# Kernel optimization log

Hardware: AMD Instinct MI355X
Metric: run time of the kernel (lower is better)

The kernel has to match this reference:

```python
import jax, jax.numpy as jnp
import numpy as np

N_QUBITS = 4
N_LAYERS = 3
SHORT_W = 2048
LONG_W = 8192
BATCH = 2048


def _conv1d(x, w, b, pad):
    # x: [B, Cin, L], w: [Cout, Cin, K]
    y = jax.lax.conv_general_dilated(x, w, window_strides=(1,), padding=[(pad, pad)],
                                     dimension_numbers=("NCH", "OIH", "NCH"))
    return y + b[None, :, None]


def _ry_mat(t):
    c, s = jnp.cos(t / 2), jnp.sin(t / 2)
    return jnp.stack([jnp.stack([c, -s]), jnp.stack([s, c])]).astype(jnp.complex64)


def _rz_mat(a):
    return jnp.diag(jnp.stack([jnp.exp(-0.5j * a), jnp.exp(0.5j * a)])).astype(jnp.complex64)


def _rot_mat(phi, theta, omega):
    # PennyLane Rot(phi, theta, omega) = RZ(omega) @ RY(theta) @ RZ(phi)
    return _rz_mat(omega) @ _ry_mat(theta) @ _rz_mat(phi)


def _apply_1q(state, U, wire):
    state = jnp.tensordot(U, state, axes=((1,), (wire,)))
    return jnp.moveaxis(state, 0, wire)


def _apply_cnot(state, c, t):
    s0 = jax.lax.index_in_dim(state, 0, axis=c, keepdims=True)
    s1 = jax.lax.index_in_dim(state, 1, axis=c, keepdims=True)
    s1 = jnp.flip(s1, axis=t)
    return jnp.concatenate([s0, s1], axis=c)


def _circuit(x, w):
    # x: [4] real features, w: [3, 4, 3] StronglyEntanglingLayers weights
    state = jnp.zeros((2,) * N_QUBITS, jnp.complex64).at[(0,) * N_QUBITS].set(1.0)
    for i in range(N_QUBITS):
        state = _apply_1q(state, _ry_mat(jnp.pi * x[i]), i)
    for l in range(N_LAYERS):
        r = (l % (N_QUBITS - 1)) + 1  # default PennyLane ranges: 1,2,3
        for i in range(N_QUBITS):
            state = _apply_1q(state, _rot_mat(w[l, i, 0], w[l, i, 1], w[l, i, 2]), i)
        for i in range(N_QUBITS):
            state = _apply_cnot(state, i, (i + r) % N_QUBITS)
    probs = jnp.abs(state) ** 2
    zs = []
    for i in range(N_QUBITS):
        p = probs.sum(axis=tuple(a for a in range(N_QUBITS) if a != i))
        zs.append(p[0] - p[1])  # <PauliZ_i>
    return jnp.stack(zs)


def setup_inputs() -> dict:
    key = jax.random.key(0)
    ks = jax.random.split(key, 13)
    d = {}
    d["xs"] = jax.random.normal(ks[0], (BATCH, 1, SHORT_W), jnp.float32)
    d["xl"] = jax.random.normal(ks[1], (BATCH, 1, LONG_W), jnp.float32)
    d["cs_conv_w"] = jax.random.normal(ks[2], (8, 1, 3), jnp.float32) * 0.3
    d["cs_conv_b"] = jax.random.normal(ks[3], (8,), jnp.float32) * 0.1
    d["cs_lin_w"] = jax.random.normal(ks[4], (2, 8 * SHORT_W), jnp.float32) * (1.0 / np.sqrt(8 * SHORT_W))
    d["cs_lin_b"] = jax.random.normal(ks[5], (2,), jnp.float32) * 0.1
    d["cl_conv_w"] = jax.random.normal(ks[6], (8, 1, 5), jnp.float32) * 0.3
    d["cl_conv_b"] = jax.random.normal(ks[7], (8,), jnp.float32) * 0.1
    d["cl_lin_w"] = jax.random.normal(ks[8], (2, 8 * LONG_W // 2), jnp.float32) * (1.0 / np.sqrt(8 * LONG_W // 2))
    d["cl_lin_b"] = jax.random.normal(ks[9], (2,), jnp.float32) * 0.1
    d["rw"] = jax.random.normal(ks[10], (N_LAYERS, N_QUBITS, 3), jnp.float32)
    d["fc_w"] = jax.random.normal(ks[11], (1, N_QUBITS), jnp.float32) * 0.5
    d["fc_b"] = jax.random.normal(ks[12], (1,), jnp.float32) * 0.1
    return d


def reference(xs, xl, cs_conv_w, cs_conv_b, cs_lin_w, cs_lin_b,
              cl_conv_w, cl_conv_b, cl_lin_w, cl_lin_b, rw, fc_w, fc_b):
    B = xs.shape[0]
    # short branch: conv(k=3,p=1) -> relu -> flatten -> linear
    hs = jax.nn.relu(_conv1d(xs, cs_conv_w, cs_conv_b, 1)).reshape(B, -1)
    fs = hs @ cs_lin_w.T + cs_lin_b  # [B, 2]
    # long branch: conv(k=5,p=2) -> relu -> maxpool(2) -> flatten -> linear
    hl = jax.nn.relu(_conv1d(xl, cl_conv_w, cl_conv_b, 2))
    hl = hl.reshape(B, 8, LONG_W // 2, 2).max(axis=-1).reshape(B, -1)
    fl = hl @ cl_lin_w.T + cl_lin_b  # [B, 2]
    f = jnp.concatenate([fs, fl], axis=1)  # [B, 4]
    # original detaches features before the quantum circuit
    f = jax.lax.stop_gradient(f)
    rw_c = jax.lax.stop_gradient(rw)
    qo = jax.vmap(lambda x: _circuit(x, rw_c))(f).astype(jnp.float32)  # [B, 4]
    return qo @ fc_w.T + fc_b  # [B, 1]
```

## Files before the change

kernel.cpp:

```cpp
#include <hip/hip_runtime.h>
#include <math.h>

namespace {
constexpr int kB  = 2048;
constexpr int kSW = 2048;
constexpr int kLW = 8192;
constexpr int kLP = kLW / 2;
constexpr int kROWS = 4;
constexpr int kNBLK = 3072;
}

__device__ __forceinline__ void pin(float& x) { asm volatile("" : "+v"(x)); }

__device__ __forceinline__ void long_quarter(
    int blk, int q, const float* __restrict__ xl, const float* __restrict__ cw,
    const float* __restrict__ cb, const float* __restrict__ lw,
    float* __restrict__ partL) {
  __shared__ float red[kROWS][2][4];
  const int tid = threadIdx.x;
  const int b0 = blk * kROWS;

  float wgt[8][5], bias[8];
#pragma unroll
  for (int c = 0; c < 8; ++c) {
#pragma unroll
    for (int k = 0; k < 5; ++k) wgt[c][k] = cw[c * 5 + k];
    bias[c] = cb[c];
  }

  const int p0 = q * 1024 + tid * 4;
  const int s  = 2 * p0;

  float la[8][4], lbv[8][4];
#pragma unroll
  for (int c = 0; c < 8; ++c) {
    float4 a4 = *reinterpret_cast<const float4*>(lw + (size_t)c * kLP + p0);
    float4 b4 = *reinterpret_cast<const float4*>(lw + (size_t)(8 + c) * kLP + p0);
    la[c][0] = a4.x; la[c][1] = a4.y; la[c][2] = a4.z; la[c][3] = a4.w;
    lbv[c][0] = b4.x; lbv[c][1] = b4.y; lbv[c][2] = b4.z; lbv[c][3] = b4.w;
  }
#pragma unroll
  for (int c = 0; c < 8; ++c)
#pragma unroll
    for (int u = 0; u < 4; ++u) { pin(la[c][u]); pin(lbv[c][u]); }

  float acc[kROWS][2];
#pragma unroll
  for (int r = 0; r < kROWS; ++r) { acc[r][0] = 0.f; acc[r][1] = 0.f; }

#pragma unroll
  for (int g = 0; g < 2; ++g) {
    float w[2][12];
#pragma unroll
    for (int r = 0; r < 2; ++r) {
      const float* x = xl + (size_t)(b0 + g * 2 + r) * kLW;
      float2 hm = (p0 > 0) ? *reinterpret_cast<const float2*>(x + s - 2)
                           : make_float2(0.f, 0.f);
      float4 f0 = *reinterpret_cast<const float4*>(x + s);
      float4 f1 = *reinterpret_cast<const float4*>(x + s + 4);
      float2 f2 = (s + 8 < kLW) ? *reinterpret_cast<const float2*>(x + s + 8)
                                : make_float2(0.f, 0.f);
      w[r][0] = hm.x; w[r][1] = hm.y;
      w[r][2] = f0.x; w[r][3] = f0.y; w[r][4] = f0.z; w[r][5] = f0.w;
      w[r][6] = f1.x; w[r][7] = f1.y; w[r][8] = f1.z; w[r][9] = f1.w;
      w[r][10] = f2.x; w[r][11] = f2.y;
    }
#pragma unroll
    for (int r = 0; r < 2; ++r)
#pragma unroll
      for (int k = 0; k < 12; ++k) pin(w[r][k]);

#pragma unroll
    for (int c = 0; c < 8; ++c) {
#pragma unroll
      for (int r = 0; r < 2; ++r) {
        const int rr = g * 2 + r;
#pragma unroll
        for (int u = 0; u < 4; ++u) {
          float v0 = fmaf(wgt[c][0], w[r][2 * u + 0],
                     fmaf(wgt[c][1], w[r][2 * u + 1],
                     fmaf(wgt[c][2], w[r][2 * u + 2],
                     fmaf(wgt[c][3], w[r][2 * u + 3],
                     fmaf(wgt[c][4], w[r][2 * u + 4], bias[c])))));
          float v1 = fmaf(wgt[c][0], w[r][2 * u + 1],
                     fmaf(wgt[c][1], w[r][2 * u + 2],
                     fmaf(wgt[c][2], w[r][2 * u + 3],
                     fmaf(wgt[c][3], w[r][2 * u + 4],
                     fmaf(wgt[c][4], w[r][2 * u + 5], bias[c])))));
          const float m = fmaxf(fmaxf(v0, v1), 0.f);
          acc[rr][0] = fmaf(m, la[c][u], acc[rr][0]);
          acc[rr][1] = fmaf(m, lbv[c][u], acc[rr][1]);
        }
      }
    }
  }

#pragma unroll
  for (int r = 0; r < kROWS; ++r)
#pragma unroll
    for (int o = 0; o < 2; ++o) {
      float a = acc[r][o];
#pragma unroll
      for (int off = 32; off > 0; off >>= 1) a += __shfl_down(a, off);
      if ((tid & 63) == 0) red[r][o][tid >> 6] = a;
    }
  __syncthreads();
  if (tid < kROWS * 2) {
    const int r = tid >> 1, o = tid & 1;
    partL[(size_t)q * kB * 2 + (size_t)(b0 + r) * 2 + o] =
        red[r][o][0] + red[r][o][1] + red[r][o][2] + red[r][o][3];
  }
}

__device__ __forceinline__ void short_half(
    int blk, int h, const float* __restrict__ xs, const float* __restrict__ cw,
    const float* __restrict__ cb, const float* __restrict__ lw,
    float* __restrict__ partS) {
  __shared__ float red[kROWS][2][4];
  const int tid = threadIdx.x;
  const int b0 = blk * kROWS;

  float wgt[8][3], bias[8];
#pragma unroll
  for (int c = 0; c < 8; ++c) {
#pragma unroll
    for (int k = 0; k < 3; ++k) wgt[c][k] = cw[c * 3 + k];
    bias[c] = cb[c];
  }

  const int p0 = h * 1024 + tid * 4;

  float la[8][4], lbv[8][4];
#pragma unroll
  for (int c = 0; c < 8; ++c) {
    float4 a4 = *reinterpret_cast<const float4*>(lw + (size_t)c * kSW + p0);
    float4 b4 = *reinterpret_cast<const float4*>(lw + (size_t)(8 + c) * kSW + p0);
    la[c][0] = a4.x; la[c][1] = a4.y; la[c][2] = a4.z; la[c][3] = a4.w;
    lbv[c][0] = b4.x; lbv[c][1] = b4.y; lbv[c][2] = b4.z; lbv[c][3] = b4.w;
  }
#pragma unroll
  for (int c = 0; c < 8; ++c)
#pragma unroll
    for (int u = 0; u < 4; ++u) { pin(la[c][u]); pin(lbv[c][u]); }

  float w[kROWS][6];
#pragma unroll
  for (int r = 0; r < kROWS; ++r) {
    const float* x = xs + (size_t)(b0 + r) * kSW;
    float xm = (p0 > 0) ? x[p0 - 1] : 0.f;
    float4 f0 = *reinterpret_cast<const float4*>(x + p0);
    float xp = (p0 + 4 < kSW) ? x[p0 + 4] : 0.f;
    w[r][0] = xm;
    w[r][1] = f0.x; w[r][2] = f0.y; w[r][3] = f0.z; w[r][4] = f0.w;
    w[r][5] = xp;
  }
#pragma unroll
  for (int r = 0; r < kROWS; ++r)
#pragma unroll
    for (int k = 0; k < 6; ++k) pin(w[r][k]);

  float acc[kROWS][2];
#pragma unroll
  for (int r = 0; r < kROWS; ++r) { acc[r][0] = 0.f; acc[r][1] = 0.f; }

#pragma unroll
  for (int c = 0; c < 8; ++c) {
#pragma unroll
    for (int r = 0; r < kROWS; ++r) {
#pragma unroll
      for (int u = 0; u < 4; ++u) {
        float v = fmaf(wgt[c][0], w[r][u],
                  fmaf(wgt[c][1], w[r][u + 1],
                  fmaf(wgt[c][2], w[r][u + 2], bias[c])));
        const float m = fmaxf(v, 0.f);
        acc[r][0] = fmaf(m, la[c][u], acc[r][0]);
        acc[r][1] = fmaf(m, lbv[c][u], acc[r][1]);
      }
    }
  }

#pragma unroll
  for (int r = 0; r < kROWS; ++r)
#pragma unroll
    for (int o = 0; o < 2; ++o) {
      float a = acc[r][o];
#pragma unroll
      for (int off = 32; off > 0; off >>= 1) a += __shfl_down(a, off);
      if ((tid & 63) == 0) red[r][o][tid >> 6] = a;
    }
  __syncthreads();
  if (tid < kROWS * 2) {
    const int r = tid >> 1, o = tid & 1;
    partS[(size_t)h * kB * 2 + (size_t)(b0 + r) * 2 + o] =
        red[r][o][0] + red[r][o][1] + red[r][o][2] + red[r][o][3];
  }
}

__global__ __launch_bounds__(256, 3) void features_kernel(
    const float* __restrict__ xs, const float* __restrict__ cs_cw,
    const float* __restrict__ cs_cb, const float* __restrict__ cs_lw,
    const float* __restrict__ xl, const float* __restrict__ cl_cw,
    const float* __restrict__ cl_cb, const float* __restrict__ cl_lw,
    float* __restrict__ partS, float* __restrict__ partL) {
  const int bid = blockIdx.x;
  const int tri = bid / 3, rem = bid % 3;
  if (rem < 2) {
    const int li = tri * 2 + rem;
    long_quarter(li >> 2, li & 3, xl, cl_cw, cl_cb, cl_lw, partL);
  } else {
    const int si = tri;
    short_half(si >> 1, si & 1, xs, cs_cw, cs_cb, cs_lw, partS);
  }
}

template <int MASK>
__device__ __forceinline__ void apply_1q(float (&ar)[16], float (&ai)[16],
                                         float u00r, float u00i, float u01r, float u01i,
                                         float u10r, float u10i, float u11r, float u11i) {
#pragma unroll
  for (int i = 0; i < 16; ++i) {
    if (!(i & MASK)) {
      const int j = i | MASK;
      const float a0r = ar[i], a0i = ai[i];
      const float a1r = ar[j], a1i = ai[j];
      ar[i] = u00r * a0r - u00i * a0i + u01r * a1r - u01i * a1i;
      ai[i] = u00r * a0i + u00i * a0r + u01r * a1i + u01i * a1r;
      ar[j] = u10r * a0r - u10i * a0i + u11r * a1r - u11i * a1i;
      ai[j] = u10r * a0i + u10i * a0r + u11r * a1i + u11i * a1r;
    }
  }
}

template <int MASK>
__device__ __forceinline__ void apply_ry(float (&ar)[16], float (&ai)[16], float half_t) {
  float s, c;
  sincosf(half_t, &s, &c);
  apply_1q<MASK>(ar, ai, c, 0.f, -s, 0.f, s, 0.f, c, 0.f);
}

template <int MASK>
__device__ __forceinline__ void apply_rot(float (&ar)[16], float (&ai)[16],
                                          float phi, float theta, float omega) {
  float st, ct; sincosf(0.5f * theta, &st, &ct);
  float sa, ca; sincosf(0.5f * (phi + omega), &sa, &ca);
  float sm, cm; sincosf(0.5f * (phi - omega), &sm, &cm);
  apply_1q<MASK>(ar, ai,
                 ct * ca, -ct * sa,
                 -st * cm, -st * sm,
                 st * cm, -st * sm,
                 ct * ca, ct * sa);
}

template <int MC, int MT>
__device__ __forceinline__ void apply_cnot(float (&ar)[16], float (&ai)[16]) {
#pragma unroll
  for (int i = 0; i < 16; ++i) {
    if ((i & MC) && !(i & MT)) {
      const int j = i | MT;
      float t;
      t = ar[i]; ar[i] = ar[j]; ar[j] = t;
      t = ai[i]; ai[i] = ai[j]; ai[j] = t;
    }
  }
}

__global__ __launch_bounds__(64) void quantum_kernel(
    const float* __restrict__ partS, const float* __restrict__ partL,
    const float* __restrict__ cs_lb, const float* __restrict__ cl_lb,
    const float* __restrict__ rw, const float* __restrict__ fcw,
    const float* __restrict__ fcb, float* __restrict__ out) {
  const int b = blockIdx.x * 64 + threadIdx.x;
  if (b >= kB) return;

  const float f0 = partS[(size_t)b * 2 + 0] + partS[(size_t)kB * 2 + b * 2 + 0] + cs_lb[0];
  const float f1 = partS[(size_t)b * 2 + 1] + partS[(size_t)kB * 2 + b * 2 + 1] + cs_lb[1];
  float f2 = cl_lb[0], f3 = cl_lb[1];
#pragma unroll
  for (int q = 0; q < 4; ++q) {
    f2 += partL[(size_t)q * kB * 2 + b * 2 + 0];
    f3 += partL[(size_t)q * kB * 2 + b * 2 + 1];
  }

  float ar[16], ai[16];
#pragma unroll
  for (int i = 0; i < 16; ++i) { ar[i] = 0.f; ai[i] = 0.f; }
  ar[0] = 1.f;

  const float kHalfPi = 1.57079632679489662f;
  apply_ry<8>(ar, ai, kHalfPi * f0);
  apply_ry<4>(ar, ai, kHalfPi * f1);
  apply_ry<2>(ar, ai, kHalfPi * f2);
  apply_ry<1>(ar, ai, kHalfPi * f3);

  apply_rot<8>(ar, ai, rw[0], rw[1], rw[2]);
  apply_rot<4>(ar, ai, rw[3], rw[4], rw[5]);
  apply_rot<2>(ar, ai, rw[6], rw[7], rw[8]);
  apply_rot<1>(ar, ai, rw[9], rw[10], rw[11]);
  apply_cnot<8, 4>(ar, ai);
  apply_cnot<4, 2>(ar, ai);
  apply_cnot<2, 1>(ar, ai);
  apply_cnot<1, 8>(ar, ai);

  apply_rot<8>(ar, ai, rw[12], rw[13], rw[14]);
  apply_rot<4>(ar, ai, rw[15], rw[16], rw[17]);
  apply_rot<2>(ar, ai, rw[18], rw[19], rw[20]);
  apply_rot<1>(ar, ai, rw[21], rw[22], rw[23]);
  apply_cnot<8, 2>(ar, ai);
  apply_cnot<4, 1>(ar, ai);
  apply_cnot<2, 8>(ar, ai);
  apply_cnot<1, 4>(ar, ai);

  apply_rot<8>(ar, ai, rw[24], rw[25], rw[26]);
  apply_rot<4>(ar, ai, rw[27], rw[28], rw[29]);
  apply_rot<2>(ar, ai, rw[30], rw[31], rw[32]);
  apply_rot<1>(ar, ai, rw[33], rw[34], rw[35]);
  apply_cnot<8, 1>(ar, ai);
  apply_cnot<4, 8>(ar, ai);
  apply_cnot<2, 4>(ar, ai);
  apply_cnot<1, 2>(ar, ai);

  float z0 = 0.f, z1 = 0.f, z2 = 0.f, z3 = 0.f;
#pragma unroll
  for (int i = 0; i < 16; ++i) {
    const float p = ar[i] * ar[i] + ai[i] * ai[i];
    z0 += (i & 8) ? -p : p;
    z1 += (i & 4) ? -p : p;
    z2 += (i & 2) ? -p : p;
    z3 += (i & 1) ? -p : p;
  }
  out[b] = fcb[0] + z0 * fcw[0] + z1 * fcw[1] + z2 * fcw[2] + z3 * fcw[3];
}

extern "C" void kernel_launch(void* const* d_in, const int* in_sizes, int n_in,
                              void* d_out, int out_size, void* d_ws, size_t ws_size,
                              hipStream_t stream) {
  const float* xs     = (const float*)d_in[0];
  const float* xl     = (const float*)d_in[1];
  const float* cs_cw  = (const float*)d_in[2];
  const float* cs_cb  = (const float*)d_in[3];
  const float* cs_lw  = (const float*)d_in[4];
  const float* cs_lb  = (const float*)d_in[5];
  const float* cl_cw  = (const float*)d_in[6];
  const float* cl_cb  = (const float*)d_in[7];
  const float* cl_lw  = (const float*)d_in[8];
  const float* cl_lb  = (const float*)d_in[9];
  const float* rw     = (const float*)d_in[10];
  const float* fcw    = (const float*)d_in[11];
  const float* fcb    = (const float*)d_in[12];
  float* out   = (float*)d_out;
  float* partS = (float*)d_ws;
  float* partL = (float*)d_ws + 2 * kB * 2;

  hipLaunchKernelGGL(features_kernel, dim3(kNBLK), dim3(256), 0, stream,
                     xs, cs_cw, cs_cb, cs_lw,
                     xl, cl_cw, cl_cb, cl_lw, partS, partL);
  hipLaunchKernelGGL(quantum_kernel, dim3(kB / 64), dim3(64), 0, stream,
                     partS, partL, cs_lb, cl_lb, rw, fcw, fcb, out);
}
```

Before: 54.84 us.

## Shrink feature blocks to one wave looping over four chunks

Each feature block drops from 256 threads to a single 64-lane wavefront, which walks four 256-element chunks in a loop instead of spreading them across four waves. The cross-wave shared-memory reduction and __syncthreads go away, leaving only a wave shuffle reduction with lane 0 writing the results. Linear weights are now reloaded per chunk instead of pinned in registers, and the asm register pins are removed. The cost is less parallelism per block, plus longer serial loops that may expose more memory latency per wave.

```diff
diff --git a/kernel.cpp b/kernel.cpp
--- a/kernel.cpp
+++ b/kernel.cpp
@@ -10,14 +10,11 @@
 constexpr int kNBLK = 3072;
 }
 
-__device__ __forceinline__ void pin(float& x) { asm volatile("" : "+v"(x)); }
-
 __device__ __forceinline__ void long_quarter(
     int blk, int q, const float* __restrict__ xl, const float* __restrict__ cw,
     const float* __restrict__ cb, const float* __restrict__ lw,
     float* __restrict__ partL) {
-  __shared__ float red[kROWS][2][4];
-  const int tid = threadIdx.x;
+  const int lane = threadIdx.x;
   const int b0 = blk * kROWS;
 
   float wgt[8][5], bias[8];
@@ -28,32 +25,18 @@
     bias[c] = cb[c];
   }
 
-  const int p0 = q * 1024 + tid * 4;
-  const int s  = 2 * p0;
-
-  float la[8][4], lbv[8][4];
-#pragma unroll
-  for (int c = 0; c < 8; ++c) {
-    float4 a4 = *reinterpret_cast<const float4*>(lw + (size_t)c * kLP + p0);
-    float4 b4 = *reinterpret_cast<const float4*>(lw + (size_t)(8 + c) * kLP + p0);
-    la[c][0] = a4.x; la[c][1] = a4.y; la[c][2] = a4.z; la[c][3] = a4.w;
-    lbv[c][0] = b4.x; lbv[c][1] = b4.y; lbv[c][2] = b4.z; lbv[c][3] = b4.w;
-  }
-#pragma unroll
-  for (int c = 0; c < 8; ++c)
-#pragma unroll
-    for (int u = 0; u < 4; ++u) { pin(la[c][u]); pin(lbv[c][u]); }
-
   float acc[kROWS][2];
 #pragma unroll
   for (int r = 0; r < kROWS; ++r) { acc[r][0] = 0.f; acc[r][1] = 0.f; }
 
-#pragma unroll
-  for (int g = 0; g < 2; ++g) {
-    float w[2][12];
-#pragma unroll
-    for (int r = 0; r < 2; ++r) {
-      const float* x = xl + (size_t)(b0 + g * 2 + r) * kLW;
+  for (int ch = 0; ch < 4; ++ch) {
+    const int p0 = q * 1024 + ch * 256 + lane * 4;
+    const int s  = 2 * p0;
+
+    float w[kROWS][12];
+#pragma unroll
+    for (int r = 0; r < kROWS; ++r) {
+      const float* x = xl + (size_t)(b0 + r) * kLW;
       float2 hm = (p0 > 0) ? *reinterpret_cast<const float2*>(x + s - 2)
                            : make_float2(0.f, 0.f);
       float4 f0 = *reinterpret_cast<const float4*>(x + s);
@@ -65,16 +48,19 @@
       w[r][6] = f1.x; w[r][7] = f1.y; w[r][8] = f1.z; w[r][9] = f1.w;
       w[r][10] = f2.x; w[r][11] = f2.y;
     }
-#pragma unroll
-    for (int r = 0; r < 2; ++r)
-#pragma unroll
-      for (int k = 0; k < 12; ++k) pin(w[r][k]);
-
+    float4 la4[8], lb4[8];
 #pragma unroll
     for (int c = 0; c < 8; ++c) {
-#pragma unroll
-      for (int r = 0; r < 2; ++r) {
-        const int rr = g * 2 + r;
+      la4[c] = *reinterpret_cast<const float4*>(lw + (size_t)c * kLP + p0);
+      lb4[c] = *reinterpret_cast<const float4*>(lw + (size_t)(8 + c) * kLP + p0);
+    }
+
+#pragma unroll
+    for (int c = 0; c < 8; ++c) {
+      const float la[4] = {la4[c].x, la4[c].y, la4[c].z, la4[c].w};
+      const float lbv[4] = {lb4[c].x, lb4[c].y, lb4[c].z, lb4[c].w};
+#pragma unroll
+      for (int r = 0; r < kROWS; ++r) {
 #pragma unroll
         for (int u = 0; u < 4; ++u) {
           float v0 = fmaf(wgt[c][0], w[r][2 * u + 0],
@@ -88,8 +74,8 @@
                      fmaf(wgt[c][3], w[r][2 * u + 4],
                      fmaf(wgt[c][4], w[r][2 * u + 5], bias[c])))));
           const float m = fmaxf(fmaxf(v0, v1), 0.f);
-          acc[rr][0] = fmaf(m, la[c][u], acc[rr][0]);
-          acc[rr][1] = fmaf(m, lbv[c][u], acc[rr][1]);
+          acc[r][0] = fmaf(m, la[u], acc[r][0]);
+          acc[r][1] = fmaf(m, lbv[u], acc[r][1]);
         }
       }
     }
@@ -99,16 +85,16 @@
   for (int r = 0; r < kROWS; ++r)
 #pragma unroll
     for (int o = 0; o < 2; ++o) {
-      float a = acc[r][o];
-#pragma unroll
-      for (int off = 32; off > 0; off >>= 1) a += __shfl_down(a, off);
-      if ((tid & 63) == 0) red[r][o][tid >> 6] = a;
-    }
-  __syncthreads();
-  if (tid < kROWS * 2) {
-    const int r = tid >> 1, o = tid & 1;
-    partL[(size_t)q * kB * 2 + (size_t)(b0 + r) * 2 + o] =
-        red[r][o][0] + red[r][o][1] + red[r][o][2] + red[r][o][3];
+#pragma unroll
+      for (int off = 32; off > 0; off >>= 1)
+        acc[r][o] += __shfl_down(acc[r][o], off);
+    }
+  if (lane == 0) {
+#pragma unroll
+    for (int r = 0; r < kROWS; ++r) {
+      partL[(size_t)q * kB * 2 + (size_t)(b0 + r) * 2 + 0] = acc[r][0];
+      partL[(size_t)q * kB * 2 + (size_t)(b0 + r) * 2 + 1] = acc[r][1];
+    }
   }
 }
 
@@ -116,8 +102,7 @@
     int blk, int h, const float* __restrict__ xs, const float* __restrict__ cw,
     const float* __restrict__ cb, const float* __restrict__ lw,
     float* __restrict__ partS) {
-  __shared__ float red[kROWS][2][4];
-  const int tid = threadIdx.x;
+  const int lane = threadIdx.x;
   const int b0 = blk * kROWS;
 
   float wgt[8][3], bias[8];
@@ -128,75 +113,68 @@
     bias[c] = cb[c];
   }
 
-  const int p0 = h * 1024 + tid * 4;
-
-  float la[8][4], lbv[8][4];
-#pragma unroll
-  for (int c = 0; c < 8; ++c) {
-    float4 a4 = *reinterpret_cast<const float4*>(lw + (size_t)c * kSW + p0);
-    float4 b4 = *reinterpret_cast<const float4*>(lw + (size_t)(8 + c) * kSW + p0);
-    la[c][0] = a4.x; la[c][1] = a4.y; la[c][2] = a4.z; la[c][3] = a4.w;
-    lbv[c][0] = b4.x; lbv[c][1] = b4.y; lbv[c][2] = b4.z; lbv[c][3] = b4.w;
-  }
-#pragma unroll
-  for (int c = 0; c < 8; ++c)
-#pragma unroll
-    for (int u = 0; u < 4; ++u) { pin(la[c][u]); pin(lbv[c][u]); }
-
-  float w[kROWS][6];
-#pragma unroll
-  for (int r = 0; r < kROWS; ++r) {
-    const float* x = xs + (size_t)(b0 + r) * kSW;
-    float xm = (p0 > 0) ? x[p0 - 1] : 0.f;
-    float4 f0 = *reinterpret_cast<const float4*>(x + p0);
-    float xp = (p0 + 4 < kSW) ? x[p0 + 4] : 0.f;
-    w[r][0] = xm;
-    w[r][1] = f0.x; w[r][2] = f0.y; w[r][3] = f0.z; w[r][4] = f0.w;
-    w[r][5] = xp;
-  }
+  float acc[kROWS][2];
+#pragma unroll
+  for (int r = 0; r < kROWS; ++r) { acc[r][0] = 0.f; acc[r][1] = 0.f; }
+
+  for (int ch = 0; ch < 4; ++ch) {
+    const int p0 = h * 1024 + ch * 256 + lane * 4;
+
+    float w[kROWS][6];
+#pragma unroll
+    for (int r = 0; r < kROWS; ++r) {
+      const float* x = xs + (size_t)(b0 + r) * kSW;
+      float xm = (p0 > 0) ? x[p0 - 1] : 0.f;
+      float4 f0 = *reinterpret_cast<const float4*>(x + p0);
+      float xp = (p0 + 4 < kSW) ? x[p0 + 4] : 0.f;
+      w[r][0] = xm;
+      w[r][1] = f0.x; w[r][2] = f0.y; w[r][3] = f0.z; w[r][4] = f0.w;
+      w[r][5] = xp;
+    }
+    float4 la4[8], lb4[8];
+#pragma unroll
+    for (int c = 0; c < 8; ++c) {
+      la4[c] = *reinterpret_cast<const float4*>(lw + (size_t)c * kSW + p0);
+      lb4[c] = *reinterpret_cast<const float4*>(lw + (size_t)(8 + c) * kSW + p0);
+    }
+
+#pragma unroll
+    for (int c = 0; c < 8; ++c) {
+      const float la[4] = {la4[c].x, la4[c].y, la4[c].z, la4[c].w};
+      const float lbv[4] = {lb4[c].x, lb4[c].y, lb4[c].z, lb4[c].w};
+#pragma unroll
+      for (int r = 0; r < kROWS; ++r) {
+#pragma unroll
+        for (int u = 0; u < 4; ++u) {
+          float v = fmaf(wgt[c][0], w[r][u],
+                    fmaf(wgt[c][1], w[r][u + 1],
+                    fmaf(wgt[c][2], w[r][u + 2], bias[c])));
+          const float m = fmaxf(v, 0.f);
+          acc[r][0] = fmaf(m, la[u], acc[r][0]);
+          acc[r][1] = fmaf(m, lbv[u], acc[r][1]);
+        }
+      }
+    }
+  }
+
 #pragma unroll
   for (int r = 0; r < kROWS; ++r)
 #pragma unroll
-    for (int k = 0; k < 6; ++k) pin(w[r][k]);
-
-  float acc[kROWS][2];
-#pragma unroll
-  for (int r = 0; r < kROWS; ++r) { acc[r][0] = 0.f; acc[r][1] = 0.f; }
-
-#pragma unroll
-  for (int c = 0; c < 8; ++c) {
+    for (int o = 0; o < 2; ++o) {
+#pragma unroll
+      for (int off = 32; off > 0; off >>= 1)
+        acc[r][o] += __shfl_down(acc[r][o], off);
+    }
+  if (lane == 0) {
 #pragma unroll
     for (int r = 0; r < kROWS; ++r) {
-#pragma unroll
-      for (int u = 0; u < 4; ++u) {
-        float v = fmaf(wgt[c][0], w[r][u],
-                  fmaf(wgt[c][1], w[r][u + 1],
-                  fmaf(wgt[c][2], w[r][u + 2], bias[c])));
-        const float m = fmaxf(v, 0.f);
-        acc[r][0] = fmaf(m, la[c][u], acc[r][0]);
-        acc[r][1] = fmaf(m, lbv[c][u], acc[r][1]);
-      }
-    }
-  }
-
-#pragma unroll
-  for (int r = 0; r < kROWS; ++r)
-#pragma unroll
-    for (int o = 0; o < 2; ++o) {
-      float a = acc[r][o];
-#pragma unroll
-      for (int off = 32; off > 0; off >>= 1) a += __shfl_down(a, off);
-      if ((tid & 63) == 0) red[r][o][tid >> 6] = a;
-    }
-  __syncthreads();
-  if (tid < kROWS * 2) {
-    const int r = tid >> 1, o = tid & 1;
-    partS[(size_t)h * kB * 2 + (size_t)(b0 + r) * 2 + o] =
-        red[r][o][0] + red[r][o][1] + red[r][o][2] + red[r][o][3];
-  }
-}
-
-__global__ __launch_bounds__(256, 3) void features_kernel(
+      partS[(size_t)h * kB * 2 + (size_t)(b0 + r) * 2 + 0] = acc[r][0];
+      partS[(size_t)h * kB * 2 + (size_t)(b0 + r) * 2 + 1] = acc[r][1];
+    }
+  }
+}
+
+__global__ __launch_bounds__(64, 4) void features_kernel(
     const float* __restrict__ xs, const float* __restrict__ cs_cw,
     const float* __restrict__ cs_cb, const float* __restrict__ cs_lw,
     const float* __restrict__ xl, const float* __restrict__ cl_cw,
@@ -351,7 +329,7 @@
   float* partS = (float*)d_ws;
   float* partL = (float*)d_ws + 2 * kB * 2;
 
-  hipLaunchKernelGGL(features_kernel, dim3(kNBLK), dim3(256), 0, stream,
+  hipLaunchKernelGGL(features_kernel, dim3(kNBLK), dim3(64), 0, stream,
                      xs, cs_cw, cs_cb, cs_lw,
                      xl, cl_cw, cl_cb, cl_lw, partS, partL);
   hipLaunchKernelGGL(quantum_kernel, dim3(kB / 64), dim3(64), 0, stream,
```

New measurement: 52.11 us. 5.0% less time.
